# Kernel tuning notes

Measured on AMD Instinct MI355X. Metric: run time of the kernel, lower is better.

Reference implementation:

```python
import jax, jax.numpy as jnp
import numpy as np

H = 128      # hidden_size
B = 8192     # number of sessions
L = 50       # items per session (constant here; code supports ragged)
T = B * L    # total tokens


def setup_inputs() -> dict:
    key = jax.random.key(0)
    ks = jax.random.split(key, 10)
    s = 1.0 / np.sqrt(H)
    u = lambda k, shape: jax.random.uniform(k, shape, jnp.float32, -s, s)
    return {
        "intra_item_emb": jax.random.normal(ks[0], (T, H), jnp.float32),
        "inter_item_emb": jax.random.normal(ks[1], (T, H), jnp.float32),
        "W1": u(ks[2], (H, H)), "b1": u(ks[3], (H,)),
        "W2": u(ks[4], (H, H)), "b2": u(ks[5], (H,)),
        "q_w": u(ks[6], (1, H)), "q_b": u(ks[7], (1,)),
        "W3": u(ks[8], (H, 2 * H)), "b3": u(ks[9], (H,)),
        "seq_len": jnp.full((B,), L, dtype=jnp.int32),
    }


def reference(intra_item_emb, inter_item_emb, W1, b1, W2, b2, q_w, q_b, W3, b3, seq_len):
    # max_fusing: elementwise max of the two embedding streams  [T, H]
    hidden = jnp.maximum(intra_item_emb, inter_item_emb)
    nB = seq_len.shape[0]
    nT = hidden.shape[0]
    # segment id per token and index of last token of each session
    seg_ids = jnp.repeat(jnp.arange(nB), seq_len, total_repeat_length=nT)  # [T]
    last_idx = jnp.cumsum(seq_len) - 1                                      # [B]
    v_n = hidden[last_idx]                 # [B, H] last node of each session
    v_n_rep = v_n[seg_ids]                 # [T, H] broadcast last node to tokens
    # attention weight per token: q(sigmoid(W1 v_n + W2 h))  [T, 1]
    alpha = jax.nn.sigmoid(v_n_rep @ W1.T + b1 + hidden @ W2.T + b2) @ q_w.T + q_b
    # segment-sum pooling of alpha-weighted tokens  [B, H]
    s_g = jax.ops.segment_sum(alpha * hidden, seg_ids, num_segments=nB)
    # final session representation  [B, H]
    h_s = jnp.concatenate([v_n, s_g], axis=1) @ W3.T + b3
    return h_s
```

## Files before the change

kernel.cpp:

```cpp
#include <hip/hip_runtime.h>
#include <hip/hip_bf16.h>

#define HDIM 128
#define RS 136

typedef __attribute__((ext_vector_type(8))) short short8;
typedef __attribute__((ext_vector_type(4))) float floatv4;

static __device__ __forceinline__ unsigned short f2bf(float f) {
  union { float f; unsigned u; } x; x.f = f;
  unsigned r = x.u + 0x7fffu + ((x.u >> 16) & 1u);
  return (unsigned short)(r >> 16);
}
static __device__ __forceinline__ float blo(unsigned u) { return __uint_as_float(u << 16); }
static __device__ __forceinline__ float bhi(unsigned u) { return __uint_as_float(u & 0xffff0000u); }

__global__ void prep_kernel(const int* __restrict__ seq, int* __restrict__ offs, int B,
                            const float* __restrict__ W1, const float* __restrict__ W2,
                            const float* __restrict__ W3,
                            unsigned short* __restrict__ w1b, unsigned short* __restrict__ w2b,
                            unsigned short* __restrict__ w3b) {
  if (blockIdx.x == 0) {
    __shared__ int part[256];
    int tid = threadIdx.x;
    int chunk = (B + 255) >> 8;
    int beg = tid * chunk, end = min(beg + chunk, B);
    int s = 0;
    for (int i = beg; i < end; ++i) s += seq[i];
    part[tid] = s;
    __syncthreads();
    for (int d = 1; d < 256; d <<= 1) {
      int v = (tid >= d) ? part[tid - d] : 0;
      __syncthreads();
      part[tid] += v;
      __syncthreads();
    }
    int run = (tid == 0) ? 0 : part[tid - 1];
    for (int i = beg; i < end; ++i) { offs[i] = run; run += seq[i]; }
  } else {
    int i = (blockIdx.x - 1) * 256 + threadIdx.x;
    if (i < 16384) { w1b[i] = f2bf(W1[i]); w2b[i] = f2bf(W2[i]); }
    if (i < 32768) { w3b[i] = f2bf(W3[i]); }
  }
}

__global__ __launch_bounds__(256) void session_kernel(
    const float* __restrict__ intra, const float* __restrict__ inter,
    const unsigned short* __restrict__ w1b, const float* __restrict__ b1,
    const unsigned short* __restrict__ w2b, const float* __restrict__ b2,
    const float* __restrict__ qw, const float* __restrict__ qb,
    const unsigned short* __restrict__ w3b, const float* __restrict__ b3,
    const int* __restrict__ seq, const int* __restrict__ offs,
    float* __restrict__ out) {
  __shared__ unsigned short hbf[64 * RS];
  __shared__ unsigned short vnb[HDIM];
  __shared__ unsigned short sgb[HDIM];
  __shared__ float alphaAcc[64];
  __shared__ float sgpart[4][HDIM];

  const int b = blockIdx.x;
  const int tid = threadIdx.x;
  const int lane = tid & 63, wid = tid >> 6;
  const int quad = lane >> 4, lcol = lane & 15;
  const int nbase = wid << 5;
  const int n0 = nbase + lcol, n1 = n0 + 16;

  int n = seq[b];
  const int start = offs[b];
  if (n > 64) n = 64;

  if (tid < HDIM) {
    int last = start + n - 1;
    if (last < 0) last = 0;
    size_t base = (size_t)last * HDIM + tid;
    vnb[tid] = f2bf(fmaxf(intra[base], inter[base]));
  }
  if (tid < 64) alphaAcc[tid] = qb[0];

  {
    const float4* pa = (const float4*)(intra + (size_t)start * HDIM);
    const float4* pb = (const float4*)(inter + (size_t)start * HDIM);
    #pragma unroll
    for (int it = 0; it < 8; ++it) {
      int idx = (it << 8) + tid;
      int t = idx >> 5, j4 = idx & 31;
      float4 r; r.x = 0.f; r.y = 0.f; r.z = 0.f; r.w = 0.f;
      if (t < n) {
        float4 a = pa[idx], c = pb[idx];
        r.x = fmaxf(a.x, c.x); r.y = fmaxf(a.y, c.y);
        r.z = fmaxf(a.z, c.z); r.w = fmaxf(a.w, c.w);
      }
      union { __hip_bfloat162 b; unsigned u; } p01, p23;
      p01.b = __float22bfloat162_rn(make_float2(r.x, r.y));
      p23.b = __float22bfloat162_rn(make_float2(r.z, r.w));
      uint2 st; st.x = p01.u; st.y = p23.u;
      *(uint2*)&hbf[t * RS + (j4 << 2)] = st;
    }
  }

  short8 w2f[2][4];
  #pragma unroll
  for (int nt = 0; nt < 2; ++nt) {
    int nn = nbase + (nt << 4) + lcol;
    #pragma unroll
    for (int kt = 0; kt < 4; ++kt)
      w2f[nt][kt] = *(const short8*)(w2b + nn * HDIM + (kt << 5) + (quad << 3));
  }
  __syncthreads();

  float c0, c1;
  {
    floatv4 p0 = {0.f, 0.f, 0.f, 0.f}, p1 = {0.f, 0.f, 0.f, 0.f};
    #pragma unroll
    for (int kt = 0; kt < 4; ++kt) {
      short8 af = *(const short8*)&vnb[(kt << 5) + (quad << 3)];
      short8 bf0 = *(const short8*)(w1b + n0 * HDIM + (kt << 5) + (quad << 3));
      short8 bf1 = *(const short8*)(w1b + n1 * HDIM + (kt << 5) + (quad << 3));
      p0 = __builtin_amdgcn_mfma_f32_16x16x32_bf16(af, bf0, p0, 0, 0, 0);
      p1 = __builtin_amdgcn_mfma_f32_16x16x32_bf16(af, bf1, p1, 0, 0, 0);
    }
    c0 = p0[0] + b1[n0] + b2[n0];
    c1 = p1[0] + b1[n1] + b2[n1];
  }
  const float q0 = qw[n0], q1 = qw[n1];

  #pragma unroll
  for (int mt = 0; mt < 4; ++mt) {
    floatv4 a0 = {c0, c0, c0, c0}, a1 = {c1, c1, c1, c1};
    const unsigned short* arow = &hbf[((mt << 4) + lcol) * RS + (quad << 3)];
    #pragma unroll
    for (int kt = 0; kt < 4; ++kt) {
      short8 af = *(const short8*)(arow + (kt << 5));
      a0 = __builtin_amdgcn_mfma_f32_16x16x32_bf16(af, w2f[0][kt], a0, 0, 0, 0);
      a1 = __builtin_amdgcn_mfma_f32_16x16x32_bf16(af, w2f[1][kt], a1, 0, 0, 0);
    }
    #pragma unroll
    for (int r = 0; r < 4; ++r) {
      float v = q0 * __builtin_amdgcn_rcpf(1.f + __expf(-a0[r]))
              + q1 * __builtin_amdgcn_rcpf(1.f + __expf(-a1[r]));
      v += __shfl_xor(v, 1, 64);
      v += __shfl_xor(v, 2, 64);
      v += __shfl_xor(v, 4, 64);
      v += __shfl_xor(v, 8, 64);
      if (lcol == 0) atomicAdd(&alphaAcc[(mt << 4) + (quad << 2) + r], v);
    }
  }
  __syncthreads();

  {
    int jg = tid & 15, ts = tid >> 4;
    float ac[8];
    #pragma unroll
    for (int e = 0; e < 8; ++e) ac[e] = 0.f;
    #pragma unroll
    for (int tt = 0; tt < 4; ++tt) {
      int t = (tt << 4) + ts;
      float al = alphaAcc[t];
      uint4 u = *(const uint4*)&hbf[t * RS + (jg << 3)];
      ac[0] += al * blo(u.x); ac[1] += al * bhi(u.x);
      ac[2] += al * blo(u.y); ac[3] += al * bhi(u.y);
      ac[4] += al * blo(u.z); ac[5] += al * bhi(u.z);
      ac[6] += al * blo(u.w); ac[7] += al * bhi(u.w);
    }
    #pragma unroll
    for (int e = 0; e < 8; ++e) {
      ac[e] += __shfl_xor(ac[e], 16, 64);
      ac[e] += __shfl_xor(ac[e], 32, 64);
    }
    if (quad == 0) {
      float4 s0; s0.x = ac[0]; s0.y = ac[1]; s0.z = ac[2]; s0.w = ac[3];
      float4 s1; s1.x = ac[4]; s1.y = ac[5]; s1.z = ac[6]; s1.w = ac[7];
      *(float4*)&sgpart[wid][(jg << 3)] = s0;
      *(float4*)&sgpart[wid][(jg << 3) + 4] = s1;
    }
  }
  __syncthreads();
  if (tid < HDIM) {
    float s = sgpart[0][tid] + sgpart[1][tid] + sgpart[2][tid] + sgpart[3][tid];
    sgb[tid] = f2bf(s);
  }
  __syncthreads();

  {
    floatv4 o0 = {0.f, 0.f, 0.f, 0.f}, o1 = {0.f, 0.f, 0.f, 0.f};
    #pragma unroll
    for (int kt = 0; kt < 8; ++kt) {
      const unsigned short* src = (kt < 4) ? &vnb[kt << 5] : &sgb[(kt - 4) << 5];
      short8 af = *(const short8*)(src + (quad << 3));
      short8 bf0 = *(const short8*)(w3b + n0 * 256 + (kt << 5) + (quad << 3));
      short8 bf1 = *(const short8*)(w3b + n1 * 256 + (kt << 5) + (quad << 3));
      o0 = __builtin_amdgcn_mfma_f32_16x16x32_bf16(af, bf0, o0, 0, 0, 0);
      o1 = __builtin_amdgcn_mfma_f32_16x16x32_bf16(af, bf1, o1, 0, 0, 0);
    }
    if (quad == 0) {
      out[(size_t)b * HDIM + n0] = o0[0] + b3[n0];
      out[(size_t)b * HDIM + n1] = o1[0] + b3[n1];
    }
  }
}

extern "C" void kernel_launch(void* const* d_in, const int* in_sizes, int n_in,
                              void* d_out, int out_size, void* d_ws, size_t ws_size,
                              hipStream_t stream) {
  const float* intra = (const float*)d_in[0];
  const float* inter = (const float*)d_in[1];
  const float* W1 = (const float*)d_in[2];
  const float* b1 = (const float*)d_in[3];
  const float* W2 = (const float*)d_in[4];
  const float* b2 = (const float*)d_in[5];
  const float* qw = (const float*)d_in[6];
  const float* qb = (const float*)d_in[7];
  const float* W3 = (const float*)d_in[8];
  const float* b3 = (const float*)d_in[9];
  const int* seq = (const int*)d_in[10];
  const int B = in_sizes[10];
  float* out = (float*)d_out;

  char* ws = (char*)d_ws;
  size_t o1 = (((size_t)B * 4) + 255) & ~(size_t)255;
  int* offs = (int*)ws;
  unsigned short* w1b = (unsigned short*)(ws + o1);
  unsigned short* w2b = (unsigned short*)(ws + o1 + 32768);
  unsigned short* w3b = (unsigned short*)(ws + o1 + 65536);

  hipLaunchKernelGGL(prep_kernel, dim3(129), dim3(256), 0, stream,
                     seq, offs, B, W1, W2, W3, w1b, w2b, w3b);
  hipLaunchKernelGGL(session_kernel, dim3(B), dim3(256), 0, stream,
                     intra, inter, w1b, b1, w2b, b2, qw, qb, w3b, b3, seq, offs, out);
}
```

Before: 506.3 us.

## Make session kernel persistent with register prefetch of next session's embeddings

```diff
diff --git a/kernel.cpp b/kernel.cpp
--- a/kernel.cpp
+++ b/kernel.cpp
@@ -14,6 +14,12 @@
 }
 static __device__ __forceinline__ float blo(unsigned u) { return __uint_as_float(u << 16); }
 static __device__ __forceinline__ float bhi(unsigned u) { return __uint_as_float(u & 0xffff0000u); }
+
+static __device__ __forceinline__ void sync_lds() {
+  asm volatile("s_waitcnt lgkmcnt(0)" ::: "memory");
+  __builtin_amdgcn_s_barrier();
+  asm volatile("" ::: "memory");
+}
 
 __global__ void prep_kernel(const int* __restrict__ seq, int* __restrict__ offs, int B,
                             const float* __restrict__ W1, const float* __restrict__ W2,
@@ -44,59 +50,31 @@
   }
 }
 
-__global__ __launch_bounds__(256) void session_kernel(
+__global__ __launch_bounds__(256, 3) void session_kernel(
     const float* __restrict__ intra, const float* __restrict__ inter,
     const unsigned short* __restrict__ w1b, const float* __restrict__ b1,
     const unsigned short* __restrict__ w2b, const float* __restrict__ b2,
     const float* __restrict__ qw, const float* __restrict__ qb,
     const unsigned short* __restrict__ w3b, const float* __restrict__ b3,
     const int* __restrict__ seq, const int* __restrict__ offs,
-    float* __restrict__ out) {
+    float* __restrict__ out, int B) {
   __shared__ unsigned short hbf[64 * RS];
   __shared__ unsigned short vnb[HDIM];
   __shared__ unsigned short sgb[HDIM];
   __shared__ float alphaAcc[64];
   __shared__ float sgpart[4][HDIM];
 
-  const int b = blockIdx.x;
   const int tid = threadIdx.x;
   const int lane = tid & 63, wid = tid >> 6;
   const int quad = lane >> 4, lcol = lane & 15;
   const int nbase = wid << 5;
   const int n0 = nbase + lcol, n1 = n0 + 16;
-
-  int n = seq[b];
-  const int start = offs[b];
-  if (n > 64) n = 64;
-
-  if (tid < HDIM) {
-    int last = start + n - 1;
-    if (last < 0) last = 0;
-    size_t base = (size_t)last * HDIM + tid;
-    vnb[tid] = f2bf(fmaxf(intra[base], inter[base]));
-  }
-  if (tid < 64) alphaAcc[tid] = qb[0];
-
-  {
-    const float4* pa = (const float4*)(intra + (size_t)start * HDIM);
-    const float4* pb = (const float4*)(inter + (size_t)start * HDIM);
-    #pragma unroll
-    for (int it = 0; it < 8; ++it) {
-      int idx = (it << 8) + tid;
-      int t = idx >> 5, j4 = idx & 31;
-      float4 r; r.x = 0.f; r.y = 0.f; r.z = 0.f; r.w = 0.f;
-      if (t < n) {
-        float4 a = pa[idx], c = pb[idx];
-        r.x = fmaxf(a.x, c.x); r.y = fmaxf(a.y, c.y);
-        r.z = fmaxf(a.z, c.z); r.w = fmaxf(a.w, c.w);
-      }
-      union { __hip_bfloat162 b; unsigned u; } p01, p23;
-      p01.b = __float22bfloat162_rn(make_float2(r.x, r.y));
-      p23.b = __float22bfloat162_rn(make_float2(r.z, r.w));
-      uint2 st; st.x = p01.u; st.y = p23.u;
-      *(uint2*)&hbf[t * RS + (j4 << 2)] = st;
-    }
-  }
+  const int G = gridDim.x;
+
+  const float qb0 = qb[0];
+  const float bb0 = b1[n0] + b2[n0], bb1 = b1[n1] + b2[n1];
+  const float q0 = qw[n0], q1 = qw[n1];
+  const float b30 = b3[n0], b31 = b3[n1];
 
   short8 w2f[2][4];
   #pragma unroll
@@ -106,96 +84,151 @@
     for (int kt = 0; kt < 4; ++kt)
       w2f[nt][kt] = *(const short8*)(w2b + nn * HDIM + (kt << 5) + (quad << 3));
   }
-  __syncthreads();
-
-  float c0, c1;
+
+  float4 ra[8], rb[8];
+  int n_cur;
   {
-    floatv4 p0 = {0.f, 0.f, 0.f, 0.f}, p1 = {0.f, 0.f, 0.f, 0.f};
-    #pragma unroll
-    for (int kt = 0; kt < 4; ++kt) {
-      short8 af = *(const short8*)&vnb[(kt << 5) + (quad << 3)];
-      short8 bf0 = *(const short8*)(w1b + n0 * HDIM + (kt << 5) + (quad << 3));
-      short8 bf1 = *(const short8*)(w1b + n1 * HDIM + (kt << 5) + (quad << 3));
-      p0 = __builtin_amdgcn_mfma_f32_16x16x32_bf16(af, bf0, p0, 0, 0, 0);
-      p1 = __builtin_amdgcn_mfma_f32_16x16x32_bf16(af, bf1, p1, 0, 0, 0);
-    }
-    c0 = p0[0] + b1[n0] + b2[n0];
-    c1 = p1[0] + b1[n1] + b2[n1];
-  }
-  const float q0 = qw[n0], q1 = qw[n1];
-
-  #pragma unroll
-  for (int mt = 0; mt < 4; ++mt) {
-    floatv4 a0 = {c0, c0, c0, c0}, a1 = {c1, c1, c1, c1};
-    const unsigned short* arow = &hbf[((mt << 4) + lcol) * RS + (quad << 3)];
-    #pragma unroll
-    for (int kt = 0; kt < 4; ++kt) {
-      short8 af = *(const short8*)(arow + (kt << 5));
-      a0 = __builtin_amdgcn_mfma_f32_16x16x32_bf16(af, w2f[0][kt], a0, 0, 0, 0);
-      a1 = __builtin_amdgcn_mfma_f32_16x16x32_bf16(af, w2f[1][kt], a1, 0, 0, 0);
-    }
-    #pragma unroll
-    for (int r = 0; r < 4; ++r) {
-      float v = q0 * __builtin_amdgcn_rcpf(1.f + __expf(-a0[r]))
-              + q1 * __builtin_amdgcn_rcpf(1.f + __expf(-a1[r]));
-      v += __shfl_xor(v, 1, 64);
-      v += __shfl_xor(v, 2, 64);
-      v += __shfl_xor(v, 4, 64);
-      v += __shfl_xor(v, 8, 64);
-      if (lcol == 0) atomicAdd(&alphaAcc[(mt << 4) + (quad << 2) + r], v);
-    }
-  }
-  __syncthreads();
-
-  {
-    int jg = tid & 15, ts = tid >> 4;
-    float ac[8];
-    #pragma unroll
-    for (int e = 0; e < 8; ++e) ac[e] = 0.f;
-    #pragma unroll
-    for (int tt = 0; tt < 4; ++tt) {
-      int t = (tt << 4) + ts;
-      float al = alphaAcc[t];
-      uint4 u = *(const uint4*)&hbf[t * RS + (jg << 3)];
-      ac[0] += al * blo(u.x); ac[1] += al * bhi(u.x);
-      ac[2] += al * blo(u.y); ac[3] += al * bhi(u.y);
-      ac[4] += al * blo(u.z); ac[5] += al * bhi(u.z);
-      ac[6] += al * blo(u.w); ac[7] += al * bhi(u.w);
-    }
-    #pragma unroll
-    for (int e = 0; e < 8; ++e) {
-      ac[e] += __shfl_xor(ac[e], 16, 64);
-      ac[e] += __shfl_xor(ac[e], 32, 64);
-    }
-    if (quad == 0) {
-      float4 s0; s0.x = ac[0]; s0.y = ac[1]; s0.z = ac[2]; s0.w = ac[3];
-      float4 s1; s1.x = ac[4]; s1.y = ac[5]; s1.z = ac[6]; s1.w = ac[7];
-      *(float4*)&sgpart[wid][(jg << 3)] = s0;
-      *(float4*)&sgpart[wid][(jg << 3) + 4] = s1;
-    }
-  }
-  __syncthreads();
-  if (tid < HDIM) {
-    float s = sgpart[0][tid] + sgpart[1][tid] + sgpart[2][tid] + sgpart[3][tid];
-    sgb[tid] = f2bf(s);
-  }
-  __syncthreads();
-
-  {
-    floatv4 o0 = {0.f, 0.f, 0.f, 0.f}, o1 = {0.f, 0.f, 0.f, 0.f};
-    #pragma unroll
-    for (int kt = 0; kt < 8; ++kt) {
-      const unsigned short* src = (kt < 4) ? &vnb[kt << 5] : &sgb[(kt - 4) << 5];
-      short8 af = *(const short8*)(src + (quad << 3));
-      short8 bf0 = *(const short8*)(w3b + n0 * 256 + (kt << 5) + (quad << 3));
-      short8 bf1 = *(const short8*)(w3b + n1 * 256 + (kt << 5) + (quad << 3));
-      o0 = __builtin_amdgcn_mfma_f32_16x16x32_bf16(af, bf0, o0, 0, 0, 0);
-      o1 = __builtin_amdgcn_mfma_f32_16x16x32_bf16(af, bf1, o1, 0, 0, 0);
-    }
-    if (quad == 0) {
-      out[(size_t)b * HDIM + n0] = o0[0] + b3[n0];
-      out[(size_t)b * HDIM + n1] = o1[0] + b3[n1];
-    }
+    int s0 = blockIdx.x;
+    n_cur = seq[s0]; if (n_cur > 64) n_cur = 64;
+    int st0 = offs[s0];
+    const float4* pa = (const float4*)(intra + (size_t)st0 * HDIM);
+    const float4* pb = (const float4*)(inter + (size_t)st0 * HDIM);
+    #pragma unroll
+    for (int it = 0; it < 8; ++it) {
+      int idx = (it << 8) + tid, t = idx >> 5;
+      float4 z; z.x = 0.f; z.y = 0.f; z.z = 0.f; z.w = 0.f;
+      float4 va = z, vb = z;
+      if (t < n_cur) { va = pa[idx]; vb = pb[idx]; }
+      ra[it] = va; rb[it] = vb;
+    }
+  }
+
+  for (int s = blockIdx.x; s < B; s += G) {
+    const int sn = s + G;
+    int n_nxt = 0, st_nxt = 0;
+    if (sn < B) { n_nxt = seq[sn]; if (n_nxt > 64) n_nxt = 64; st_nxt = offs[sn]; }
+
+    const int lastrow = (n_cur > 0) ? (n_cur - 1) : 0;
+    #pragma unroll
+    for (int it = 0; it < 8; ++it) {
+      int idx = (it << 8) + tid;
+      int t = idx >> 5, j4 = idx & 31;
+      float4 a = ra[it], c = rb[it];
+      union { __hip_bfloat162 b; unsigned u; } p01, p23;
+      p01.b = __float22bfloat162_rn(make_float2(fmaxf(a.x, c.x), fmaxf(a.y, c.y)));
+      p23.b = __float22bfloat162_rn(make_float2(fmaxf(a.z, c.z), fmaxf(a.w, c.w)));
+      uint2 st; st.x = p01.u; st.y = p23.u;
+      *(uint2*)&hbf[t * RS + (j4 << 2)] = st;
+      if (t == lastrow) *(uint2*)&vnb[j4 << 2] = st;
+    }
+    if (tid < 64) alphaAcc[tid] = qb0;
+    sync_lds();
+
+    float c0, c1;
+    {
+      floatv4 p0 = {0.f, 0.f, 0.f, 0.f}, p1 = {0.f, 0.f, 0.f, 0.f};
+      #pragma unroll
+      for (int kt = 0; kt < 4; ++kt) {
+        short8 af = *(const short8*)&vnb[(kt << 5) + (quad << 3)];
+        short8 bf0 = *(const short8*)(w1b + n0 * HDIM + (kt << 5) + (quad << 3));
+        short8 bf1 = *(const short8*)(w1b + n1 * HDIM + (kt << 5) + (quad << 3));
+        p0 = __builtin_amdgcn_mfma_f32_16x16x32_bf16(af, bf0, p0, 0, 0, 0);
+        p1 = __builtin_amdgcn_mfma_f32_16x16x32_bf16(af, bf1, p1, 0, 0, 0);
+      }
+      c0 = p0[0] + bb0;
+      c1 = p1[0] + bb1;
+    }
+
+    if (sn < B) {
+      const float4* pa = (const float4*)(intra + (size_t)st_nxt * HDIM);
+      const float4* pb = (const float4*)(inter + (size_t)st_nxt * HDIM);
+      #pragma unroll
+      for (int it = 0; it < 8; ++it) {
+        int idx = (it << 8) + tid, t = idx >> 5;
+        float4 z; z.x = 0.f; z.y = 0.f; z.z = 0.f; z.w = 0.f;
+        float4 va = z, vb = z;
+        if (t < n_nxt) { va = pa[idx]; vb = pb[idx]; }
+        ra[it] = va; rb[it] = vb;
+      }
+    }
+    asm volatile("" ::: "memory");
+
+    #pragma unroll
+    for (int mt = 0; mt < 4; ++mt) {
+      floatv4 a0 = {c0, c0, c0, c0}, a1 = {c1, c1, c1, c1};
+      const unsigned short* arow = &hbf[((mt << 4) + lcol) * RS + (quad << 3)];
+      #pragma unroll
+      for (int kt = 0; kt < 4; ++kt) {
+        short8 af = *(const short8*)(arow + (kt << 5));
+        a0 = __builtin_amdgcn_mfma_f32_16x16x32_bf16(af, w2f[0][kt], a0, 0, 0, 0);
+        a1 = __builtin_amdgcn_mfma_f32_16x16x32_bf16(af, w2f[1][kt], a1, 0, 0, 0);
+      }
+      #pragma unroll
+      for (int r = 0; r < 4; ++r) {
+        float v = q0 * __builtin_amdgcn_rcpf(1.f + __expf(-a0[r]))
+                + q1 * __builtin_amdgcn_rcpf(1.f + __expf(-a1[r]));
+        v += __shfl_xor(v, 1, 64);
+        v += __shfl_xor(v, 2, 64);
+        v += __shfl_xor(v, 4, 64);
+        v += __shfl_xor(v, 8, 64);
+        if (lcol == 0) atomicAdd(&alphaAcc[(mt << 4) + (quad << 2) + r], v);
+      }
+    }
+    sync_lds();
+
+    {
+      int jg = tid & 15, ts = tid >> 4;
+      float ac[8];
+      #pragma unroll
+      for (int e = 0; e < 8; ++e) ac[e] = 0.f;
+      #pragma unroll
+      for (int tt = 0; tt < 4; ++tt) {
+        int t = (tt << 4) + ts;
+        float al = alphaAcc[t];
+        uint4 u = *(const uint4*)&hbf[t * RS + (jg << 3)];
+        ac[0] += al * blo(u.x); ac[1] += al * bhi(u.x);
+        ac[2] += al * blo(u.y); ac[3] += al * bhi(u.y);
+        ac[4] += al * blo(u.z); ac[5] += al * bhi(u.z);
+        ac[6] += al * blo(u.w); ac[7] += al * bhi(u.w);
+      }
+      #pragma unroll
+      for (int e = 0; e < 8; ++e) {
+        ac[e] += __shfl_xor(ac[e], 16, 64);
+        ac[e] += __shfl_xor(ac[e], 32, 64);
+      }
+      if (quad == 0) {
+        float4 s0v; s0v.x = ac[0]; s0v.y = ac[1]; s0v.z = ac[2]; s0v.w = ac[3];
+        float4 s1v; s1v.x = ac[4]; s1v.y = ac[5]; s1v.z = ac[6]; s1v.w = ac[7];
+        *(float4*)&sgpart[wid][(jg << 3)] = s0v;
+        *(float4*)&sgpart[wid][(jg << 3) + 4] = s1v;
+      }
+    }
+    sync_lds();
+    if (tid < HDIM) {
+      float sv = sgpart[0][tid] + sgpart[1][tid] + sgpart[2][tid] + sgpart[3][tid];
+      sgb[tid] = f2bf(sv);
+    }
+    sync_lds();
+
+    {
+      floatv4 o0 = {0.f, 0.f, 0.f, 0.f}, o1 = {0.f, 0.f, 0.f, 0.f};
+      #pragma unroll
+      for (int kt = 0; kt < 8; ++kt) {
+        const unsigned short* src = (kt < 4) ? &vnb[kt << 5] : &sgb[(kt - 4) << 5];
+        short8 af = *(const short8*)(src + (quad << 3));
+        short8 bf0 = *(const short8*)(w3b + n0 * 256 + (kt << 5) + (quad << 3));
+        short8 bf1 = *(const short8*)(w3b + n1 * 256 + (kt << 5) + (quad << 3));
+        o0 = __builtin_amdgcn_mfma_f32_16x16x32_bf16(af, bf0, o0, 0, 0, 0);
+        o1 = __builtin_amdgcn_mfma_f32_16x16x32_bf16(af, bf1, o1, 0, 0, 0);
+      }
+      if (quad == 0) {
+        out[(size_t)s * HDIM + n0] = o0[0] + b30;
+        out[(size_t)s * HDIM + n1] = o1[0] + b31;
+      }
+    }
+    sync_lds();
+
+    n_cur = n_nxt;
   }
 }
 
@@ -223,8 +256,10 @@
   unsigned short* w2b = (unsigned short*)(ws + o1 + 32768);
   unsigned short* w3b = (unsigned short*)(ws + o1 + 65536);
 
+  int nblk = B < 2048 ? B : 2048;
+
   hipLaunchKernelGGL(prep_kernel, dim3(129), dim3(256), 0, stream,
                      seq, offs, B, W1, W2, W3, w1b, w2b, w3b);
-  hipLaunchKernelGGL(session_kernel, dim3(B), dim3(256), 0, stream,
-                     intra, inter, w1b, b1, w2b, b2, qw, qb, w3b, b3, seq, offs, out);
-}
+  hipLaunchKernelGGL(session_kernel, dim3(nblk), dim3(256), 0, stream,
+                     intra, inter, w1b, b1, w2b, b2, qw, qb, w3b, b3, seq, offs, out, B);
+}
```

Result: slower. 563.8 us (+11.4%).
